# Kernel tuning notes

Hardware: AMD Instinct MI355X
Metric: run time of the kernel (lower is better)

Reference implementation:

```python
import jax, jax.numpy as jnp
import numpy as np

NJ = 12
# shift buffer: inverse of the fixed 12x12 permutation matrix (= its transpose)
_idx = np.array([0, 1, 6, 2, 3, 8, 9, 7, 4, 5, 10, 11])
_P = np.zeros((NJ, NJ), np.float32)
_P[np.arange(NJ), _idx] = 1.0
SHIFT = jnp.asarray(_P.T)


def _bn(x, g, b, eps=1e-5):
    # BatchNorm2d in training mode: biased var over (batch, positions) per channel
    m = x.mean(axis=(0, 1), keepdims=True)
    v = x.var(axis=(0, 1), keepdims=True)
    return (x - m) * jax.lax.rsqrt(v + eps) * g + b


def setup_inputs() -> dict:
    key = jax.random.key(0)
    ks = jax.random.split(key, 10)
    B, D, E = 16384, 128, 128
    Din = D + E
    f32 = jnp.float32
    inp = {
        "gout": jax.random.normal(ks[0], (B, NJ, D), f32),
        "eout": jax.random.normal(ks[1], (B, NJ, E), f32),
        "ev_shift": jax.random.uniform(ks[2], (NJ, NJ), f32),
        "ve_shift": jax.random.uniform(ks[3], (NJ, NJ), f32),
        "W_ev": jax.random.normal(ks[4], (D, Din), f32) * 0.001,
        "W_ve": jax.random.normal(ks[5], (D, Din), f32) * 0.001,
        "W1": jax.random.normal(ks[6], (D, 3 * D), f32) * 0.001,
        "W2": jax.random.normal(ks[7], (D, 3 * D), f32) * 0.001,
        "W3": jax.random.normal(ks[8], (D, 2 * D), f32) * 0.001,
        "W4": jax.random.normal(ks[9], (D, 3 * D), f32) * 0.001,
    }
    for name in ["ev", "ve", "1", "2", "3", "4"]:
        inp["g_" + name] = jnp.ones((D,), f32)
        inp["b_" + name] = jnp.zeros((D,), f32)
    return inp


def reference(gout, eout, ev_shift, ve_shift, W_ev, g_ev, b_ev, W_ve, g_ve, b_ve,
              W1, g_1, b_1, W2, g_2, b_2, W3, g_3, b_3, W4, g_4, b_4):
    # gout: [B, 12, D], eout: [B, 12, E]
    ev_g = jnp.einsum('ij,bjd->bid', ev_shift, gout)
    ve_g = jnp.einsum('ij,bjd->bid', ve_shift, gout)
    # conv1x1 over channel dim == linear over feature dim; BN stats over (B, joints)
    ef = jax.nn.relu(_bn(jnp.einsum('bnc,dc->bnd', jnp.concatenate([eout, ev_g], -1), W_ev), g_ev, b_ev))
    vf = jax.nn.relu(_bn(jnp.einsum('bnc,dc->bnd', jnp.concatenate([ve_g, eout], -1), W_ve), g_ve, b_ve))
    # node_res blocks: per-group gather+concat -> linear -> BN (stats over B*group_positions)
    op1 = _bn(jnp.concatenate([ef[:, 0], ef[:, 1], ef[:, 5]], -1)[:, None] @ W1.T, g_1, b_1)
    op2_in = jnp.stack([
        jnp.concatenate([vf[:, 0], ef[:, 3], ef[:, 7]], -1),
        jnp.concatenate([vf[:, 5], ef[:, 7], ef[:, 8]], -1)], axis=1)
    op2 = _bn(op2_in @ W2.T, g_2, b_2)
    op3_in = jnp.stack([
        jnp.concatenate([vf[:, 1], ef[:, 2]], -1),
        jnp.concatenate([vf[:, 3], ef[:, 4]], -1),
        jnp.concatenate([vf[:, 8], ef[:, 9]], -1),
        jnp.concatenate([vf[:, 10], ef[:, 11]], -1)], axis=1)
    op3 = _bn(op3_in @ W3.T, g_3, b_3)
    op4 = _bn(jnp.concatenate([vf[:, 6], vf[:, 7], ef[:, 10]], -1)[:, None] @ W4.T, g_4, b_4)
    op5 = jnp.stack([vf[:, 2], vf[:, 4], vf[:, 9], vf[:, 11]], axis=1)
    res = jnp.concatenate([op1, op2, op3, op4, op5], axis=1)  # [B, 12, D]
    res = jnp.einsum('ij,bjd->bid', SHIFT, res)
    return jax.nn.relu(gout + res)
```

## Files before the change

kernel.cpp:

```cpp
#include <hip/hip_runtime.h>
#include <hip/hip_bf16.h>

#define BTOT 16384
typedef unsigned short u16;
typedef __attribute__((ext_vector_type(8))) short bf16x8;
typedef __attribute__((ext_vector_type(8))) unsigned short u16x8;
typedef __attribute__((ext_vector_type(4))) float f32x4;

#define MFMA16(a, b, c) __builtin_amdgcn_mfma_f32_16x16x32_bf16(a, b, c, 0, 0, 0)
#define NSLOT 16

__device__ __forceinline__ u16 f2b(float f) {
  unsigned int i = __float_as_uint(f);
  return (u16)((i + 0x7FFFu + ((i >> 16) & 1u)) >> 16);
}
__device__ __forceinline__ float b2f(u16 u) {
  return __uint_as_float(((unsigned int)u) << 16);
}
__device__ __forceinline__ unsigned pk2(float x, float y) {
  __hip_bfloat162 h = __float22bfloat162_rn(make_float2(x, y));
  unsigned r; __builtin_memcpy(&r, &h, 4); return r;
}
__device__ __forceinline__ bf16x8 pack8(float4 lo, float4 hi) {
  union { unsigned u[4]; bf16x8 v; } r;
  r.u[0] = pk2(lo.x, lo.y); r.u[1] = pk2(lo.z, lo.w);
  r.u[2] = pk2(hi.x, hi.y); r.u[3] = pk2(hi.z, hi.w);
  return r.v;
}

__device__ const int c_mb[8][3]  = {{0,0,0},{1,0,0},{1,0,0},{1,0,0},{1,0,0},{1,0,0},{1,0,0},{1,1,0}};
__device__ const int c_mj[8][3]  = {{0,1,5},{0,3,7},{5,7,8},{1,2,0},{3,4,0},{8,9,0},{10,11,0},{6,7,10}};
__device__ const int c_opof[8]   = {0,1,1,2,2,2,2,3};
__device__ const int c_jmap[12]  = {0,1,3,4,8,9,2,7,5,6,10,11};
__device__ const int c_vj[4]     = {2,4,9,11};

__global__ __launch_bounds__(256) void k_prep(
    const float* __restrict__ wev, const float* __restrict__ wve,
    const float* __restrict__ w1, const float* __restrict__ w2,
    const float* __restrict__ w3, const float* __restrict__ w4,
    u16* __restrict__ wb, float* __restrict__ stats)
{
  int id = blockIdx.x * 256 + threadIdx.x;
  if (blockIdx.x == 0) {
    for (int i = threadIdx.x; i < NSLOT * 1536; i += 256) stats[i] = 0.f;
  }
  const float* src; int base, K, local;
  if (id < 32768)       { src = wev; base = 0;      K = 256; local = id; }
  else if (id < 65536)  { src = wve; base = 32768;  K = 256; local = id - 32768; }
  else if (id < 114688) { src = w1;  base = 65536;  K = 384; local = id - 65536; }
  else if (id < 163840) { src = w2;  base = 114688; K = 384; local = id - 114688; }
  else if (id < 196608) { src = w3;  base = 163840; K = 256; local = id - 163840; }
  else if (id < 245760) { src = w4;  base = 196608; K = 384; local = id - 196608; }
  else return;
  int d = local / K, k = local - d * K;
  int dk = (base == 32768) ? (k ^ 128) : k;
  int dest = base + (dk >> 6) * 8192 + d * 64 + ((dk & 63) ^ ((d & 7) << 3));
  wb[dest] = f2b(src[local]);
}

__global__ __launch_bounds__(256, 2) void k_stage1(
    const float* __restrict__ gout, const float* __restrict__ eout,
    const float* __restrict__ evs, const float* __restrict__ ves,
    const u16* __restrict__ wb_ev, const u16* __restrict__ wb_ve,
    u16* __restrict__ y_ev, u16* __restrict__ y_ve, float* __restrict__ stats)
{
  __shared__ __align__(16) char lds[81920];
  char* se = lds;
  char* sm = lds + 24576;
  char* sw = lds + 49152;
  float* s_red = (float*)(lds + 49152);

  const int tid = threadIdx.x;
  const int l = tid & 63, wv = tid >> 6;
  const int wm = wv >> 1, wn = wv & 1;
  const int b0 = blockIdx.x * 8;
  const int kq = (l >> 4) * 8;
  const int bb = tid >> 5;
  const int d4 = (tid & 31) * 4;

  u16x8 wreg[4];
  auto wload = [&](const u16* wmat, int c) {
    #pragma unroll
    for (int q = 0; q < 4; ++q)
      wreg[q] = *(const u16x8*)&wmat[c * 8192 + tid * 8 + q * 2048];
  };
  auto wstore = [&](char* buf) {
    #pragma unroll
    for (int q = 0; q < 4; ++q)
      *(u16x8*)(buf + (tid * 8 + q * 2048) * 2) = wreg[q];
  };

  wload(wb_ev, 0);

  {
    float mev[12][4];
    #pragma unroll
    for (int n = 0; n < 12; ++n)
      #pragma unroll
      for (int q = 0; q < 4; ++q) mev[n][q] = 0.f;
    #pragma unroll
    for (int j = 0; j < 12; ++j) {
      float4 g4 = *(const float4*)&gout[((size_t)(b0 + bb) * 12 + j) * 128 + d4];
      float4 e4 = *(const float4*)&eout[((size_t)(b0 + bb) * 12 + j) * 128 + d4];
      int row = bb * 12 + j;
      uint2 ep = make_uint2(pk2(e4.x, e4.y), pk2(e4.z, e4.w));
      *(uint2*)(se + row * 256 + ((d4 * 2) ^ ((row & 7) << 4))) = ep;
      #pragma unroll
      for (int n = 0; n < 12; ++n) {
        float w = evs[n * 12 + j];
        mev[n][0] = fmaf(w, g4.x, mev[n][0]); mev[n][1] = fmaf(w, g4.y, mev[n][1]);
        mev[n][2] = fmaf(w, g4.z, mev[n][2]); mev[n][3] = fmaf(w, g4.w, mev[n][3]);
      }
    }
    #pragma unroll
    for (int n = 0; n < 12; ++n) {
      int row = bb * 12 + n;
      uint2 mp = make_uint2(pk2(mev[n][0], mev[n][1]), pk2(mev[n][2], mev[n][3]));
      *(uint2*)(sm + row * 256 + ((d4 * 2) ^ ((row & 7) << 4))) = mp;
    }
  }

  float sE[4] = {0,0,0,0}, qE[4] = {0,0,0,0}, sV[4] = {0,0,0,0}, qV[4] = {0,0,0,0};

  auto run_pass = [&](const u16* wmat, const u16* nextw, u16* yout, char* dump,
                      float* sS, float* qS) {
    f32x4 acc[3][4];
    #pragma unroll
    for (int mi = 0; mi < 3; ++mi)
      #pragma unroll
      for (int ni = 0; ni < 4; ++ni) acc[mi][ni] = (f32x4){0.f, 0.f, 0.f, 0.f};

    wstore(sw);
    for (int c = 0; c < 4; ++c) {
      if (c < 3) wload(wmat, c + 1);
      else if (nextw) wload(nextw, 0);
      __syncthreads();
      const char* xb = (c < 2) ? se : sm;
      const char* swb = sw + ((c & 1) ? 16384 : 0);
      #pragma unroll
      for (int kt = 0; kt < 2; ++kt) {
        bf16x8 a[3], bq[4];
        const int kb = (((c & 1) * 64 + kt * 32 + kq)) * 2;
        #pragma unroll
        for (int mi = 0; mi < 3; ++mi) {
          int row = (wm * 3 + mi) * 16 + (l & 15);
          a[mi] = *(const bf16x8*)(xb + row * 256 + (kb ^ ((row & 7) << 4)));
        }
        const int kw = (kt * 32 + kq) * 2;
        #pragma unroll
        for (int ni = 0; ni < 4; ++ni) {
          int n = (wn * 4 + ni) * 16 + (l & 15);
          bq[ni] = *(const bf16x8*)(swb + n * 128 + (kw ^ ((n & 7) << 4)));
        }
        #pragma unroll
        for (int mi = 0; mi < 3; ++mi)
          #pragma unroll
          for (int ni = 0; ni < 4; ++ni)
            acc[mi][ni] = MFMA16(a[mi], bq[ni], acc[mi][ni]);
      }
      if (c < 3) wstore(sw + (((c + 1) & 1) ? 16384 : 0));
    }
    __syncthreads();
    #pragma unroll
    for (int mi = 0; mi < 3; ++mi)
      #pragma unroll
      for (int ni = 0; ni < 4; ++ni)
        #pragma unroll
        for (int q = 0; q < 4; ++q) {
          float v = acc[mi][ni][q];
          sS[ni] += v; qS[ni] += v * v;
          int row = (wm * 3 + mi) * 16 + (l >> 4) * 4 + q;
          int cb = ((wn * 4 + ni) * 16 + (l & 15)) * 2;
          *(u16*)(dump + row * 256 + (cb ^ ((row & 7) << 4))) = f2b(v);
        }
    __syncthreads();
    #pragma unroll
    for (int q = 0; q < 6; ++q) {
      int i = tid + q * 256;
      int row = i >> 4, cb = (i & 15) * 16;
      u16x8 v = *(const u16x8*)(dump + row * 256 + (cb ^ ((row & 7) << 4)));
      *(u16x8*)&yout[(size_t)(b0 * 12 + row) * 128 + (i & 15) * 8] = v;
    }
    __syncthreads();
  };

  run_pass(wb_ev, wb_ve, y_ev, sm, sE, qE);

  {
    float mve[12][4];
    #pragma unroll
    for (int n = 0; n < 12; ++n)
      #pragma unroll
      for (int q = 0; q < 4; ++q) mve[n][q] = 0.f;
    #pragma unroll
    for (int j = 0; j < 12; ++j) {
      float4 g4 = *(const float4*)&gout[((size_t)(b0 + bb) * 12 + j) * 128 + d4];
      #pragma unroll
      for (int n = 0; n < 12; ++n) {
        float w = ves[n * 12 + j];
        mve[n][0] = fmaf(w, g4.x, mve[n][0]); mve[n][1] = fmaf(w, g4.y, mve[n][1]);
        mve[n][2] = fmaf(w, g4.z, mve[n][2]); mve[n][3] = fmaf(w, g4.w, mve[n][3]);
      }
    }
    #pragma unroll
    for (int n = 0; n < 12; ++n) {
      int row = bb * 12 + n;
      uint2 mp = make_uint2(pk2(mve[n][0], mve[n][1]), pk2(mve[n][2], mve[n][3]));
      *(uint2*)(sm + row * 256 + ((d4 * 2) ^ ((row & 7) << 4))) = mp;
    }
  }

  run_pass(wb_ve, (const u16*)nullptr, y_ve, se, sV, qV);

  s_red[tid] = 0.f; s_red[tid + 256] = 0.f;
  __syncthreads();
  #pragma unroll
  for (int ni = 0; ni < 4; ++ni) {
    float a1 = sE[ni], b1 = qE[ni], a2 = sV[ni], b2 = qV[ni];
    a1 += __shfl_xor(a1, 16); a1 += __shfl_xor(a1, 32);
    b1 += __shfl_xor(b1, 16); b1 += __shfl_xor(b1, 32);
    a2 += __shfl_xor(a2, 16); a2 += __shfl_xor(a2, 32);
    b2 += __shfl_xor(b2, 16); b2 += __shfl_xor(b2, 32);
    if (l < 16) {
      int ch = (wn * 4 + ni) * 16 + l;
      atomicAdd(&s_red[ch], a1);       atomicAdd(&s_red[128 + ch], b1);
      atomicAdd(&s_red[256 + ch], a2); atomicAdd(&s_red[384 + ch], b2);
    }
  }
  __syncthreads();
  const int sb = (blockIdx.x & (NSLOT - 1)) * 1536;
  atomicAdd(&stats[sb + tid], s_red[tid]);
  atomicAdd(&stats[sb + 256 + tid], s_red[256 + tid]);
}

__global__ void k_fin1(const float* __restrict__ stats, float* __restrict__ scale,
                       const float* __restrict__ gev, const float* __restrict__ bev,
                       const float* __restrict__ gve, const float* __restrict__ bve)
{
  int t = threadIdx.x;
  int m = t >> 7, d = t & 127;
  float s = 0.f, q = 0.f;
  #pragma unroll
  for (int sl = 0; sl < NSLOT; ++sl) {
    s += stats[sl * 1536 + m * 256 + d];
    q += stats[sl * 1536 + m * 256 + 128 + d];
  }
  float cnt = (float)(BTOT * 12);
  float mean = s / cnt, var = q / cnt - mean * mean;
  float rs = rsqrtf(var + 1e-5f);
  float g = m ? gve[d] : gev[d];
  float b = m ? bve[d] : bev[d];
  float a = g * rs;
  scale[m * 256 + d] = a;
  scale[m * 256 + 128 + d] = b - mean * a;
}

__global__ __launch_bounds__(256, 4) void k_stage2(
    const u16* __restrict__ y_ev, const u16* __restrict__ y_ve,
    const float* __restrict__ scale,
    const u16* __restrict__ wb1, const u16* __restrict__ wb2,
    const u16* __restrict__ wb3, const u16* __restrict__ wb4,
    u16* __restrict__ y_op, float* __restrict__ stats)
{
  __shared__ __align__(16) u16 s_w[128 * 64];
  __shared__ __align__(16) u16 s_d[32 * 128];
  __shared__ float s_scale[512];
  __shared__ float s_red[256];
  char* sw = (char*)s_w; char* sd = (char*)s_d;

  const int tid = threadIdx.x, l = tid & 63, wv = tid >> 6;
  const int mw = wv & 1, nw = wv >> 1;
  const int r = blockIdx.x & 7;
  const int b0 = (blockIdx.x >> 3) * 32;
  const int Kr = (r >= 3 && r <= 6) ? 256 : 384;
  const u16* wr = (r == 0) ? wb1 : (r <= 2) ? wb2 : (r <= 6) ? wb3 : wb4;
  const int o = c_opof[r];
  const int j0 = c_mj[r][0], j1 = c_mj[r][1], j2 = c_mj[r][2];
  const int m0 = c_mb[r][0], m1 = c_mb[r][1], m2 = c_mb[r][2];

  for (int i = tid; i < 512; i += 256) s_scale[i] = scale[i];
  s_red[tid] = 0.f;

  f32x4 acc[4];
  #pragma unroll
  for (int ni = 0; ni < 4; ++ni) acc[ni] = (f32x4){0.f, 0.f, 0.f, 0.f};

  const int nch = Kr >> 6;
  const int kq = (l >> 4) * 8;
  const int batch = b0 + mw * 16 + (l & 15);

  for (int c = 0; c < nch; ++c) {
    #pragma unroll
    for (int q = 0; q < 4; ++q) {
      int off = tid * 8 + q * 2048;
      *(u16x8*)(sw + off * 2) = *(const u16x8*)&wr[c * 8192 + off];
    }
    __syncthreads();
    const int s = c >> 1;
    const int j = (s == 0) ? j0 : (s == 1) ? j1 : j2;
    const int mb = (s == 0) ? m0 : (s == 1) ? m1 : m2;
    const int sb = mb ? 256 : 0;
    const u16* ys = mb ? y_ve : y_ev;
    #pragma unroll
    for (int kt = 0; kt < 2; ++kt) {
      const int chan = (c & 1) * 64 + kt * 32 + kq;
      u16x8 u = *(const u16x8*)&ys[((size_t)batch * 12 + j) * 128 + chan];
      float4 a0 = *(const float4*)&s_scale[sb + chan];
      float4 a1 = *(const float4*)&s_scale[sb + chan + 4];
      float4 c0 = *(const float4*)&s_scale[sb + 128 + chan];
      float4 c1 = *(const float4*)&s_scale[sb + 128 + chan + 4];
      float4 lo, hi;
      lo.x = fmaxf(fmaf(b2f(u[0]), a0.x, c0.x), 0.f);
      lo.y = fmaxf(fmaf(b2f(u[1]), a0.y, c0.y), 0.f);
      lo.z = fmaxf(fmaf(b2f(u[2]), a0.z, c0.z), 0.f);
      lo.w = fmaxf(fmaf(b2f(u[3]), a0.w, c0.w), 0.f);
      hi.x = fmaxf(fmaf(b2f(u[4]), a1.x, c1.x), 0.f);
      hi.y = fmaxf(fmaf(b2f(u[5]), a1.y, c1.y), 0.f);
      hi.z = fmaxf(fmaf(b2f(u[6]), a1.z, c1.z), 0.f);
      hi.w = fmaxf(fmaf(b2f(u[7]), a1.w, c1.w), 0.f);
      bf16x8 afrag = pack8(lo, hi);
      const int kw = (kt * 32 + kq) * 2;
      #pragma unroll
      for (int ni = 0; ni < 4; ++ni) {
        int n = (nw * 4 + ni) * 16 + (l & 15);
        bf16x8 b = *(const bf16x8*)(sw + n * 128 + (kw ^ ((n & 7) << 4)));
        acc[ni] = MFMA16(afrag, b, acc[ni]);
      }
    }
    __syncthreads();
  }

  #pragma unroll
  for (int ni = 0; ni < 4; ++ni) {
    float s1 = 0.f, q1 = 0.f;
    #pragma unroll
    for (int q = 0; q < 4; ++q) {
      float v = acc[ni][q];
      s1 += v; q1 += v * v;
      int row = mw * 16 + (l >> 4) * 4 + q;
      int cb = ((nw * 4 + ni) * 16 + (l & 15)) * 2;
      *(u16*)(sd + row * 256 + (cb ^ ((row & 7) << 4))) = f2b(v);
    }
    s1 += __shfl_xor(s1, 16); s1 += __shfl_xor(s1, 32);
    q1 += __shfl_xor(q1, 16); q1 += __shfl_xor(q1, 32);
    if (l < 16) {
      int ch = (nw * 4 + ni) * 16 + l;
      atomicAdd(&s_red[ch], s1);
      atomicAdd(&s_red[128 + ch], q1);
    }
  }
  __syncthreads();
  #pragma unroll
  for (int q = 0; q < 2; ++q) {
    int i = tid + q * 256;
    int row = i >> 4, cb = (i & 15) * 16;
    u16x8 v = *(const u16x8*)(sd + row * 256 + (cb ^ ((row & 7) << 4)));
    *(u16x8*)&y_op[((size_t)(b0 + row) * 8 + r) * 128 + (i & 15) * 8] = v;
  }
  const int sb2 = (blockIdx.x & (NSLOT - 1)) * 1536;
  atomicAdd(&stats[sb2 + 512 + o * 256 + tid], s_red[tid]);
}

__global__ void k_fin2(const float* __restrict__ stats, float* __restrict__ scale,
    const float* __restrict__ g1, const float* __restrict__ b1,
    const float* __restrict__ g2, const float* __restrict__ b2,
    const float* __restrict__ g3, const float* __restrict__ b3,
    const float* __restrict__ g4, const float* __restrict__ b4)
{
  int t = threadIdx.x;
  int o = t >> 7, d = t & 127;
  float s = 0.f, q = 0.f;
  #pragma unroll
  for (int sl = 0; sl < NSLOT; ++sl) {
    s += stats[sl * 1536 + 512 + o * 256 + d];
    q += stats[sl * 1536 + 512 + o * 256 + 128 + d];
  }
  float cnt = (o == 0 || o == 3) ? 16384.f : (o == 1 ? 32768.f : 65536.f);
  float mean = s / cnt, var = q / cnt - mean * mean;
  float rs = rsqrtf(var + 1e-5f);
  const float* gp = (o == 0) ? g1 : (o == 1) ? g2 : (o == 2) ? g3 : g4;
  const float* bp = (o == 0) ? b1 : (o == 1) ? b2 : (o == 2) ? b3 : b4;
  float a = gp[d] * rs;
  scale[512 + o * 256 + d] = a;
  scale[512 + o * 256 + 128 + d] = bp[d] - mean * a;
}

__global__ __launch_bounds__(256) void k_stage3(
    const u16* __restrict__ y_op, const u16* __restrict__ y_ve,
    const float* __restrict__ scale, const float* __restrict__ gout,
    float* __restrict__ out)
{
  const int stride = gridDim.x * 256;
  const int total = BTOT * 12 * 32;
  for (int id = blockIdx.x * 256 + threadIdx.x; id < total; id += stride) {
    int b = id / 384;
    int rem = id - b * 384;
    int i = rem >> 5;
    int d4 = (rem & 31) * 4;
    int j = c_jmap[i];
    float4 v;
    if (j < 8) {
      ushort4 u = *(const ushort4*)&y_op[((size_t)b * 8 + j) * 128 + d4];
      int o = c_opof[j];
      float4 a4 = *(const float4*)&scale[512 + o * 256 + d4];
      float4 c4 = *(const float4*)&scale[512 + o * 256 + 128 + d4];
      v.x = fmaf(b2f(u.x), a4.x, c4.x);
      v.y = fmaf(b2f(u.y), a4.y, c4.y);
      v.z = fmaf(b2f(u.z), a4.z, c4.z);
      v.w = fmaf(b2f(u.w), a4.w, c4.w);
    } else {
      int jv = c_vj[j - 8];
      ushort4 u = *(const ushort4*)&y_ve[((size_t)b * 12 + jv) * 128 + d4];
      float4 a4 = *(const float4*)&scale[256 + d4];
      float4 c4 = *(const float4*)&scale[384 + d4];
      v.x = fmaxf(fmaf(b2f(u.x), a4.x, c4.x), 0.f);
      v.y = fmaxf(fmaf(b2f(u.y), a4.y, c4.y), 0.f);
      v.z = fmaxf(fmaf(b2f(u.z), a4.z, c4.z), 0.f);
      v.w = fmaxf(fmaf(b2f(u.w), a4.w, c4.w), 0.f);
    }
    float4 g4 = *(const float4*)&gout[((size_t)b * 12 + i) * 128 + d4];
    float4 r4;
    r4.x = fmaxf(g4.x + v.x, 0.f);
    r4.y = fmaxf(g4.y + v.y, 0.f);
    r4.z = fmaxf(g4.z + v.z, 0.f);
    r4.w = fmaxf(g4.w + v.w, 0.f);
    *(float4*)&out[((size_t)b * 12 + i) * 128 + d4] = r4;
  }
}

extern "C" void kernel_launch(void* const* d_in, const int* in_sizes, int n_in,
                              void* d_out, int out_size, void* d_ws, size_t ws_size,
                              hipStream_t stream) {
  (void)in_sizes; (void)n_in; (void)out_size; (void)ws_size;
  const float* gout = (const float*)d_in[0];
  const float* eout = (const float*)d_in[1];
  const float* evs  = (const float*)d_in[2];
  const float* ves  = (const float*)d_in[3];
  const float* wev  = (const float*)d_in[4];
  const float* wve  = (const float*)d_in[5];
  const float* w1   = (const float*)d_in[6];
  const float* w2   = (const float*)d_in[7];
  const float* w3   = (const float*)d_in[8];
  const float* w4   = (const float*)d_in[9];
  const float* g_ev = (const float*)d_in[10]; const float* b_ev = (const float*)d_in[11];
  const float* g_ve = (const float*)d_in[12]; const float* b_ve = (const float*)d_in[13];
  const float* g_1  = (const float*)d_in[14]; const float* b_1  = (const float*)d_in[15];
  const float* g_2  = (const float*)d_in[16]; const float* b_2  = (const float*)d_in[17];
  const float* g_3  = (const float*)d_in[18]; const float* b_3  = (const float*)d_in[19];
  const float* g_4  = (const float*)d_in[20]; const float* b_4  = (const float*)d_in[21];

  char* ws = (char*)d_ws;
  u16*   y_ev  = (u16*)ws;
  u16*   y_ve  = (u16*)(ws + 50331648);
  u16*   y_op  = (u16*)(ws + 100663296);
  u16*   wb    = (u16*)(ws + 134217728);
  float* stats = (float*)(ws + 134709248);
  float* scale = (float*)(ws + 134807552);

  k_prep<<<960, 256, 0, stream>>>(wev, wve, w1, w2, w3, w4, wb, stats);
  k_stage1<<<2048, 256, 0, stream>>>(gout, eout, evs, ves, wb, wb + 32768, y_ev, y_ve, stats);
  k_fin1<<<1, 256, 0, stream>>>(stats, scale, g_ev, b_ev, g_ve, b_ve);
  k_stage2<<<4096, 256, 0, stream>>>(y_ev, y_ve, scale, wb + 65536, wb + 114688, wb + 163840, wb + 196608, y_op, stats);
  k_fin2<<<1, 512, 0, stream>>>(stats, scale, g_1, b_1, g_2, b_2, g_3, b_3, g_4, b_4);
  k_stage3<<<4096, 256, 0, stream>>>(y_op, y_ve, scale, gout, (float*)d_out);
}
```

Measured before the change: 210.9 us.

## Fold BN finalize kernels into consumers, fuse shift passes, double-buffer weight prefetch

Removes the two single-block finalize kernels and has every stage2 and stage3 block recompute the BN scale and shift from the slot-partitioned stats into shared memory. This cuts two launches and the serial gaps they cause, at the cost of redundant stats reads in every block. Stage1 now computes both shift-matrix products in one pass over gout, dropping the second gout read but raising register pressure. Weight prefetch moves to two register buffers loaded two chunks ahead, and the stage3 grid is halved.

New measurement: 236.7 us. 12.2% more time.

```diff
diff --git a/kernel.cpp b/kernel.cpp
--- a/kernel.cpp
+++ b/kernel.cpp
@@ -78,26 +78,27 @@
   const int bb = tid >> 5;
   const int d4 = (tid & 31) * 4;
 
-  u16x8 wreg[4];
-  auto wload = [&](const u16* wmat, int c) {
+  u16x8 wreg[2][4];
+  auto wload = [&](int s, const u16* wmat, int c) {
     #pragma unroll
     for (int q = 0; q < 4; ++q)
-      wreg[q] = *(const u16x8*)&wmat[c * 8192 + tid * 8 + q * 2048];
+      wreg[s][q] = *(const u16x8*)&wmat[c * 8192 + tid * 8 + q * 2048];
   };
-  auto wstore = [&](char* buf) {
+  auto wstore = [&](int s, char* buf) {
     #pragma unroll
     for (int q = 0; q < 4; ++q)
-      *(u16x8*)(buf + (tid * 8 + q * 2048) * 2) = wreg[q];
+      *(u16x8*)(buf + (tid * 8 + q * 2048) * 2) = wreg[s][q];
   };
 
-  wload(wb_ev, 0);
-
+  wload(0, wb_ev, 0);
+
+  float mve[12][4];
   {
     float mev[12][4];
     #pragma unroll
     for (int n = 0; n < 12; ++n)
       #pragma unroll
-      for (int q = 0; q < 4; ++q) mev[n][q] = 0.f;
+      for (int q = 0; q < 4; ++q) { mev[n][q] = 0.f; mve[n][q] = 0.f; }
     #pragma unroll
     for (int j = 0; j < 12; ++j) {
       float4 g4 = *(const float4*)&gout[((size_t)(b0 + bb) * 12 + j) * 128 + d4];
@@ -107,9 +108,12 @@
       *(uint2*)(se + row * 256 + ((d4 * 2) ^ ((row & 7) << 4))) = ep;
       #pragma unroll
       for (int n = 0; n < 12; ++n) {
-        float w = evs[n * 12 + j];
-        mev[n][0] = fmaf(w, g4.x, mev[n][0]); mev[n][1] = fmaf(w, g4.y, mev[n][1]);
-        mev[n][2] = fmaf(w, g4.z, mev[n][2]); mev[n][3] = fmaf(w, g4.w, mev[n][3]);
+        float we = evs[n * 12 + j];
+        float wq = ves[n * 12 + j];
+        mev[n][0] = fmaf(we, g4.x, mev[n][0]); mev[n][1] = fmaf(we, g4.y, mev[n][1]);
+        mev[n][2] = fmaf(we, g4.z, mev[n][2]); mev[n][3] = fmaf(we, g4.w, mev[n][3]);
+        mve[n][0] = fmaf(wq, g4.x, mve[n][0]); mve[n][1] = fmaf(wq, g4.y, mve[n][1]);
+        mve[n][2] = fmaf(wq, g4.z, mve[n][2]); mve[n][3] = fmaf(wq, g4.w, mve[n][3]);
       }
     }
     #pragma unroll
@@ -130,11 +134,13 @@
       #pragma unroll
       for (int ni = 0; ni < 4; ++ni) acc[mi][ni] = (f32x4){0.f, 0.f, 0.f, 0.f};
 
-    wstore(sw);
+    wstore(0, sw);
+    wload(1, wmat, 1);
+    #pragma unroll
     for (int c = 0; c < 4; ++c) {
-      if (c < 3) wload(wmat, c + 1);
-      else if (nextw) wload(nextw, 0);
       __syncthreads();
+      if (c < 2) wload(c & 1, wmat, c + 2);
+      else if (c == 2 && nextw) wload(0, nextw, 0);
       const char* xb = (c < 2) ? se : sm;
       const char* swb = sw + ((c & 1) ? 16384 : 0);
       #pragma unroll
@@ -158,7 +164,7 @@
           for (int ni = 0; ni < 4; ++ni)
             acc[mi][ni] = MFMA16(a[mi], bq[ni], acc[mi][ni]);
       }
-      if (c < 3) wstore(sw + (((c + 1) & 1) ? 16384 : 0));
+      if (c < 3) wstore((c + 1) & 1, sw + (((c + 1) & 1) ? 16384 : 0));
     }
     __syncthreads();
     #pragma unroll
@@ -186,28 +192,11 @@
 
   run_pass(wb_ev, wb_ve, y_ev, sm, sE, qE);
 
-  {
-    float mve[12][4];
-    #pragma unroll
-    for (int n = 0; n < 12; ++n)
-      #pragma unroll
-      for (int q = 0; q < 4; ++q) mve[n][q] = 0.f;
-    #pragma unroll
-    for (int j = 0; j < 12; ++j) {
-      float4 g4 = *(const float4*)&gout[((size_t)(b0 + bb) * 12 + j) * 128 + d4];
-      #pragma unroll
-      for (int n = 0; n < 12; ++n) {
-        float w = ves[n * 12 + j];
-        mve[n][0] = fmaf(w, g4.x, mve[n][0]); mve[n][1] = fmaf(w, g4.y, mve[n][1]);
-        mve[n][2] = fmaf(w, g4.z, mve[n][2]); mve[n][3] = fmaf(w, g4.w, mve[n][3]);
-      }
-    }
-    #pragma unroll
-    for (int n = 0; n < 12; ++n) {
-      int row = bb * 12 + n;
-      uint2 mp = make_uint2(pk2(mve[n][0], mve[n][1]), pk2(mve[n][2], mve[n][3]));
-      *(uint2*)(sm + row * 256 + ((d4 * 2) ^ ((row & 7) << 4))) = mp;
-    }
+  #pragma unroll
+  for (int n = 0; n < 12; ++n) {
+    int row = bb * 12 + n;
+    uint2 mp = make_uint2(pk2(mve[n][0], mve[n][1]), pk2(mve[n][2], mve[n][3]));
+    *(uint2*)(sm + row * 256 + ((d4 * 2) ^ ((row & 7) << 4))) = mp;
   }
 
   run_pass(wb_ve, (const u16*)nullptr, y_ve, se, sV, qV);
@@ -233,34 +222,14 @@
   atomicAdd(&stats[sb + 256 + tid], s_red[256 + tid]);
 }
 
-__global__ void k_fin1(const float* __restrict__ stats, float* __restrict__ scale,
-                       const float* __restrict__ gev, const float* __restrict__ bev,
-                       const float* __restrict__ gve, const float* __restrict__ bve)
-{
-  int t = threadIdx.x;
-  int m = t >> 7, d = t & 127;
-  float s = 0.f, q = 0.f;
-  #pragma unroll
-  for (int sl = 0; sl < NSLOT; ++sl) {
-    s += stats[sl * 1536 + m * 256 + d];
-    q += stats[sl * 1536 + m * 256 + 128 + d];
-  }
-  float cnt = (float)(BTOT * 12);
-  float mean = s / cnt, var = q / cnt - mean * mean;
-  float rs = rsqrtf(var + 1e-5f);
-  float g = m ? gve[d] : gev[d];
-  float b = m ? bve[d] : bev[d];
-  float a = g * rs;
-  scale[m * 256 + d] = a;
-  scale[m * 256 + 128 + d] = b - mean * a;
-}
-
 __global__ __launch_bounds__(256, 4) void k_stage2(
     const u16* __restrict__ y_ev, const u16* __restrict__ y_ve,
-    const float* __restrict__ scale,
+    float* stats,
+    const float* __restrict__ gev, const float* __restrict__ bev,
+    const float* __restrict__ gve, const float* __restrict__ bve,
     const u16* __restrict__ wb1, const u16* __restrict__ wb2,
     const u16* __restrict__ wb3, const u16* __restrict__ wb4,
-    u16* __restrict__ y_op, float* __restrict__ stats)
+    u16* __restrict__ y_op)
 {
   __shared__ __align__(16) u16 s_w[128 * 64];
   __shared__ __align__(16) u16 s_d[32 * 128];
@@ -278,8 +247,25 @@
   const int j0 = c_mj[r][0], j1 = c_mj[r][1], j2 = c_mj[r][2];
   const int m0 = c_mb[r][0], m1 = c_mb[r][1], m2 = c_mb[r][2];
 
-  for (int i = tid; i < 512; i += 256) s_scale[i] = scale[i];
+  {
+    int m = tid >> 7, d = tid & 127;
+    float s = 0.f, q = 0.f;
+    #pragma unroll
+    for (int sl = 0; sl < NSLOT; ++sl) {
+      s += stats[sl * 1536 + m * 256 + d];
+      q += stats[sl * 1536 + m * 256 + 128 + d];
+    }
+    float cnt = (float)(BTOT * 12);
+    float mean = s / cnt, var = q / cnt - mean * mean;
+    float rs = rsqrtf(var + 1e-5f);
+    float g = m ? gve[d] : gev[d];
+    float b = m ? bve[d] : bev[d];
+    float a = g * rs;
+    s_scale[m * 256 + d] = a;
+    s_scale[m * 256 + 128 + d] = b - mean * a;
+  }
   s_red[tid] = 0.f;
+  __syncthreads();
 
   f32x4 acc[4];
   #pragma unroll
@@ -361,38 +347,53 @@
   atomicAdd(&stats[sb2 + 512 + o * 256 + tid], s_red[tid]);
 }
 
-__global__ void k_fin2(const float* __restrict__ stats, float* __restrict__ scale,
+__global__ __launch_bounds__(256) void k_stage3(
+    const u16* __restrict__ y_op, const u16* __restrict__ y_ve,
+    const float* __restrict__ stats,
+    const float* __restrict__ gve, const float* __restrict__ bve,
     const float* __restrict__ g1, const float* __restrict__ b1,
     const float* __restrict__ g2, const float* __restrict__ b2,
     const float* __restrict__ g3, const float* __restrict__ b3,
-    const float* __restrict__ g4, const float* __restrict__ b4)
+    const float* __restrict__ g4, const float* __restrict__ b4,
+    const float* __restrict__ gout, float* __restrict__ out)
 {
-  int t = threadIdx.x;
-  int o = t >> 7, d = t & 127;
-  float s = 0.f, q = 0.f;
-  #pragma unroll
-  for (int sl = 0; sl < NSLOT; ++sl) {
-    s += stats[sl * 1536 + 512 + o * 256 + d];
-    q += stats[sl * 1536 + 512 + o * 256 + 128 + d];
-  }
-  float cnt = (o == 0 || o == 3) ? 16384.f : (o == 1 ? 32768.f : 65536.f);
-  float mean = s / cnt, var = q / cnt - mean * mean;
-  float rs = rsqrtf(var + 1e-5f);
-  const float* gp = (o == 0) ? g1 : (o == 1) ? g2 : (o == 2) ? g3 : g4;
-  const float* bp = (o == 0) ? b1 : (o == 1) ? b2 : (o == 2) ? b3 : b4;
-  float a = gp[d] * rs;
-  scale[512 + o * 256 + d] = a;
-  scale[512 + o * 256 + 128 + d] = bp[d] - mean * a;
-}
-
-__global__ __launch_bounds__(256) void k_stage3(
-    const u16* __restrict__ y_op, const u16* __restrict__ y_ve,
-    const float* __restrict__ scale, const float* __restrict__ gout,
-    float* __restrict__ out)
-{
+  __shared__ float s_sc[1536];
+  const int tid = threadIdx.x;
+
+  for (int i = tid; i < 640; i += 256) {
+    int g = i >> 7, d = i & 127;
+    int sumoff, sqoff, dsta, dstc;
+    float cnt;
+    const float *gp, *bp;
+    if (g == 0) {
+      sumoff = 256 + d; sqoff = 384 + d;
+      dsta = 256 + d; dstc = 384 + d;
+      cnt = (float)(BTOT * 12); gp = gve; bp = bve;
+    } else {
+      int o = g - 1;
+      sumoff = 512 + o * 256 + d; sqoff = sumoff + 128;
+      dsta = 512 + o * 256 + d; dstc = dsta + 128;
+      cnt = (o == 0 || o == 3) ? 16384.f : (o == 1 ? 32768.f : 65536.f);
+      gp = (o == 0) ? g1 : (o == 1) ? g2 : (o == 2) ? g3 : g4;
+      bp = (o == 0) ? b1 : (o == 1) ? b2 : (o == 2) ? b3 : b4;
+    }
+    float s = 0.f, q = 0.f;
+    #pragma unroll
+    for (int sl = 0; sl < NSLOT; ++sl) {
+      s += stats[sl * 1536 + sumoff];
+      q += stats[sl * 1536 + sqoff];
+    }
+    float mean = s / cnt, var = q / cnt - mean * mean;
+    float rs = rsqrtf(var + 1e-5f);
+    float a = gp[d] * rs;
+    s_sc[dsta] = a;
+    s_sc[dstc] = bp[d] - mean * a;
+  }
+  __syncthreads();
+
   const int stride = gridDim.x * 256;
   const int total = BTOT * 12 * 32;
-  for (int id = blockIdx.x * 256 + threadIdx.x; id < total; id += stride) {
+  for (int id = blockIdx.x * 256 + tid; id < total; id += stride) {
     int b = id / 384;
     int rem = id - b * 384;
     int i = rem >> 5;
@@ -402,8 +403,8 @@
     if (j < 8) {
       ushort4 u = *(const ushort4*)&y_op[((size_t)b * 8 + j) * 128 + d4];
       int o = c_opof[j];
-      float4 a4 = *(const float4*)&scale[512 + o * 256 + d4];
-      float4 c4 = *(const float4*)&scale[512 + o * 256 + 128 + d4];
+      float4 a4 = *(const float4*)&s_sc[512 + o * 256 + d4];
+      float4 c4 = *(const float4*)&s_sc[512 + o * 256 + 128 + d4];
       v.x = fmaf(b2f(u.x), a4.x, c4.x);
       v.y = fmaf(b2f(u.y), a4.y, c4.y);
       v.z = fmaf(b2f(u.z), a4.z, c4.z);
@@ -411,8 +412,8 @@
     } else {
       int jv = c_vj[j - 8];
       ushort4 u = *(const ushort4*)&y_ve[((size_t)b * 12 + jv) * 128 + d4];
-      float4 a4 = *(const float4*)&scale[256 + d4];
-      float4 c4 = *(const float4*)&scale[384 + d4];
+      float4 a4 = *(const float4*)&s_sc[256 + d4];
+      float4 c4 = *(const float4*)&s_sc[384 + d4];
       v.x = fmaxf(fmaf(b2f(u.x), a4.x, c4.x), 0.f);
       v.y = fmaxf(fmaf(b2f(u.y), a4.y, c4.y), 0.f);
       v.z = fmaxf(fmaf(b2f(u.z), a4.z, c4.z), 0.f);
@@ -455,12 +456,12 @@
   u16*   y_op  = (u16*)(ws + 100663296);
   u16*   wb    = (u16*)(ws + 134217728);
   float* stats = (float*)(ws + 134709248);
-  float* scale = (float*)(ws + 134807552);
 
   k_prep<<<960, 256, 0, stream>>>(wev, wve, w1, w2, w3, w4, wb, stats);
   k_stage1<<<2048, 256, 0, stream>>>(gout, eout, evs, ves, wb, wb + 32768, y_ev, y_ve, stats);
-  k_fin1<<<1, 256, 0, stream>>>(stats, scale, g_ev, b_ev, g_ve, b_ve);
-  k_stage2<<<4096, 256, 0, stream>>>(y_ev, y_ve, scale, wb + 65536, wb + 114688, wb + 163840, wb + 196608, y_op, stats);
-  k_fin2<<<1, 512, 0, stream>>>(stats, scale, g_1, b_1, g_2, b_2, g_3, b_3, g_4, b_4);
-  k_stage3<<<4096, 256, 0, stream>>>(y_op, y_ve, scale, gout, (float*)d_out);
-}
+  k_stage2<<<4096, 256, 0, stream>>>(y_ev, y_ve, stats, g_ev, b_ev, g_ve, b_ve,
+                                     wb + 65536, wb + 114688, wb + 163840, wb + 196608, y_op);
+  k_stage3<<<2048, 256, 0, stream>>>(y_op, y_ve, stats, g_ve, b_ve,
+                                     g_1, b_1, g_2, b_2, g_3, b_3, g_4, b_4,
+                                     gout, (float*)d_out);
+}
```

## Load MFMA weight fragments directly from global memory in fragment-ordered layout

Applied to the files above, without the earlier changes.

The weight conversion kernel now writes bf16 weights in per-lane MFMA fragment order, so each lane's B operand is one contiguous 16-byte load. Stage 1 and stage 2 drop the LDS weight staging, its double buffering and most per-chunk barriers, and read B fragments straight from global memory, which should hit in L2. Stage 1 uses less LDS, so its launch bound goes from 2 to 3 blocks per CU. In exchange, every wave now issues global loads for weights inside the MFMA loop and depends on cache latency instead of LDS.

Measured after the change: 303.0 us. 1.44x slower.

```diff
diff --git a/kernel.cpp b/kernel.cpp
--- a/kernel.cpp
+++ b/kernel.cpp
@@ -54,21 +54,21 @@
   else return;
   int d = local / K, k = local - d * K;
   int dk = (base == 32768) ? (k ^ 128) : k;
-  int dest = base + (dk >> 6) * 8192 + d * 64 + ((dk & 63) ^ ((d & 7) << 3));
+  int c = dk >> 6, kt = (dk >> 5) & 1, kg = (dk >> 3) & 3, ko = dk & 7;
+  int dest = base + c * 8192 + (d >> 4) * 1024 + kt * 512 + ((kg << 4) + (d & 15)) * 8 + ko;
   wb[dest] = f2b(src[local]);
 }
 
-__global__ __launch_bounds__(256, 2) void k_stage1(
+__global__ __launch_bounds__(256, 3) void k_stage1(
     const float* __restrict__ gout, const float* __restrict__ eout,
     const float* __restrict__ evs, const float* __restrict__ ves,
     const u16* __restrict__ wb_ev, const u16* __restrict__ wb_ve,
     u16* __restrict__ y_ev, u16* __restrict__ y_ve, float* __restrict__ stats)
 {
-  __shared__ __align__(16) char lds[81920];
+  __shared__ __align__(16) char lds[49152];
+  __shared__ float s_red[512];
   char* se = lds;
   char* sm = lds + 24576;
-  char* sw = lds + 49152;
-  float* s_red = (float*)(lds + 49152);
 
   const int tid = threadIdx.x;
   const int l = tid & 63, wv = tid >> 6;
@@ -78,20 +78,6 @@
   const int bb = tid >> 5;
   const int d4 = (tid & 31) * 4;
 
-  u16x8 wreg[4];
-  auto wload = [&](const u16* wmat, int c) {
-    #pragma unroll
-    for (int q = 0; q < 4; ++q)
-      wreg[q] = *(const u16x8*)&wmat[c * 8192 + tid * 8 + q * 2048];
-  };
-  auto wstore = [&](char* buf) {
-    #pragma unroll
-    for (int q = 0; q < 4; ++q)
-      *(u16x8*)(buf + (tid * 8 + q * 2048) * 2) = wreg[q];
-  };
-
-  wload(wb_ev, 0);
-
   {
     float mev[12][4];
     #pragma unroll
@@ -122,35 +108,29 @@
 
   float sE[4] = {0,0,0,0}, qE[4] = {0,0,0,0}, sV[4] = {0,0,0,0}, qV[4] = {0,0,0,0};
 
-  auto run_pass = [&](const u16* wmat, const u16* nextw, u16* yout, char* dump,
-                      float* sS, float* qS) {
+  auto run_pass = [&](const u16* wmat, u16* yout, char* dump, float* sS, float* qS) {
     f32x4 acc[3][4];
     #pragma unroll
     for (int mi = 0; mi < 3; ++mi)
       #pragma unroll
       for (int ni = 0; ni < 4; ++ni) acc[mi][ni] = (f32x4){0.f, 0.f, 0.f, 0.f};
 
-    wstore(sw);
+    __syncthreads();
+    #pragma unroll
     for (int c = 0; c < 4; ++c) {
-      if (c < 3) wload(wmat, c + 1);
-      else if (nextw) wload(nextw, 0);
-      __syncthreads();
       const char* xb = (c < 2) ? se : sm;
-      const char* swb = sw + ((c & 1) ? 16384 : 0);
       #pragma unroll
       for (int kt = 0; kt < 2; ++kt) {
         bf16x8 a[3], bq[4];
+        const u16* wp = wmat + c * 8192 + kt * 512 + l * 8;
+        #pragma unroll
+        for (int ni = 0; ni < 4; ++ni)
+          bq[ni] = *(const bf16x8*)&wp[(wn * 4 + ni) * 1024];
         const int kb = (((c & 1) * 64 + kt * 32 + kq)) * 2;
         #pragma unroll
         for (int mi = 0; mi < 3; ++mi) {
           int row = (wm * 3 + mi) * 16 + (l & 15);
           a[mi] = *(const bf16x8*)(xb + row * 256 + (kb ^ ((row & 7) << 4)));
-        }
-        const int kw = (kt * 32 + kq) * 2;
-        #pragma unroll
-        for (int ni = 0; ni < 4; ++ni) {
-          int n = (wn * 4 + ni) * 16 + (l & 15);
-          bq[ni] = *(const bf16x8*)(swb + n * 128 + (kw ^ ((n & 7) << 4)));
         }
         #pragma unroll
         for (int mi = 0; mi < 3; ++mi)
@@ -158,7 +138,6 @@
           for (int ni = 0; ni < 4; ++ni)
             acc[mi][ni] = MFMA16(a[mi], bq[ni], acc[mi][ni]);
       }
-      if (c < 3) wstore(sw + (((c + 1) & 1) ? 16384 : 0));
     }
     __syncthreads();
     #pragma unroll
@@ -184,7 +163,7 @@
     __syncthreads();
   };
 
-  run_pass(wb_ev, wb_ve, y_ev, sm, sE, qE);
+  run_pass(wb_ev, y_ev, sm, sE, qE);
 
   {
     float mve[12][4];
@@ -210,7 +189,7 @@
     }
   }
 
-  run_pass(wb_ve, (const u16*)nullptr, y_ve, se, sV, qV);
+  run_pass(wb_ve, y_ve, se, sV, qV);
 
   s_red[tid] = 0.f; s_red[tid + 256] = 0.f;
   __syncthreads();
@@ -262,11 +241,10 @@
     const u16* __restrict__ wb3, const u16* __restrict__ wb4,
     u16* __restrict__ y_op, float* __restrict__ stats)
 {
-  __shared__ __align__(16) u16 s_w[128 * 64];
   __shared__ __align__(16) u16 s_d[32 * 128];
   __shared__ float s_scale[512];
   __shared__ float s_red[256];
-  char* sw = (char*)s_w; char* sd = (char*)s_d;
+  char* sd = (char*)s_d;
 
   const int tid = threadIdx.x, l = tid & 63, wv = tid >> 6;
   const int mw = wv & 1, nw = wv >> 1;
@@ -280,6 +258,7 @@
 
   for (int i = tid; i < 512; i += 256) s_scale[i] = scale[i];
   s_red[tid] = 0.f;
+  __syncthreads();
 
   f32x4 acc[4];
   #pragma unroll
@@ -290,12 +269,6 @@
   const int batch = b0 + mw * 16 + (l & 15);
 
   for (int c = 0; c < nch; ++c) {
-    #pragma unroll
-    for (int q = 0; q < 4; ++q) {
-      int off = tid * 8 + q * 2048;
-      *(u16x8*)(sw + off * 2) = *(const u16x8*)&wr[c * 8192 + off];
-    }
-    __syncthreads();
     const int s = c >> 1;
     const int j = (s == 0) ? j0 : (s == 1) ? j1 : j2;
     const int mb = (s == 0) ? m0 : (s == 1) ? m1 : m2;
@@ -319,16 +292,15 @@
       hi.z = fmaxf(fmaf(b2f(u[6]), a1.z, c1.z), 0.f);
       hi.w = fmaxf(fmaf(b2f(u[7]), a1.w, c1.w), 0.f);
       bf16x8 afrag = pack8(lo, hi);
-      const int kw = (kt * 32 + kq) * 2;
+      const u16* wp = wr + c * 8192 + kt * 512 + l * 8;
       #pragma unroll
       for (int ni = 0; ni < 4; ++ni) {
-        int n = (nw * 4 + ni) * 16 + (l & 15);
-        bf16x8 b = *(const bf16x8*)(sw + n * 128 + (kw ^ ((n & 7) << 4)));
+        bf16x8 b = *(const bf16x8*)&wp[(nw * 4 + ni) * 1024];
         acc[ni] = MFMA16(afrag, b, acc[ni]);
       }
     }
-    __syncthreads();
-  }
+  }
+  __syncthreads();
 
   #pragma unroll
   for (int ni = 0; ni < 4; ++ni) {
```
